# Kernel tuning notes

Hardware: AMD Instinct MI355X
Metric: run time of the kernel (lower is better)

The kernel has to match this reference:

```python
import jax, jax.numpy as jnp
import numpy as np
from functools import partial

STRIDES = (8, 16, 32)
SIZES = ((80, 80), (40, 40), (20, 20))
NUM_CLASSES = 80
NMS_THR = 0.65
SCORE_THR = 0.01
MAX_DET = 100  # fixed-size NMS output (padded; validity = scores > 0)


def setup_inputs() -> dict:
    key = jax.random.key(0)
    ks = jax.random.split(key, 9)
    B = 32
    out = {}
    for i, (h, w) in enumerate(SIZES):
        out[f"cls{i}"] = jax.random.normal(ks[3 * i], (B, NUM_CLASSES, h, w), jnp.float32)
        out[f"reg{i}"] = jax.random.normal(ks[3 * i + 1], (B, 4, h, w), jnp.float32)
        out[f"obj{i}"] = jax.random.normal(ks[3 * i + 2], (B, 1, h, w), jnp.float32)
    return out


def _grid_points():
    # MlvlPointGenerator.grid_priors(with_stride=True), offset=0: (x, y, stride, stride)
    pts = []
    for (h, w), s in zip(SIZES, STRIDES):
        xs = jnp.arange(w, dtype=jnp.float32) * s
        ys = jnp.arange(h, dtype=jnp.float32) * s
        xx, yy = jnp.meshgrid(xs, ys)  # [h, w], x varies fastest -> matches NHWC flatten
        st = jnp.full((h * w,), float(s), jnp.float32)
        pts.append(jnp.stack([xx.ravel(), yy.ravel(), st, st], axis=-1))
    return jnp.concatenate(pts, axis=0)  # [A, 4]


def _flatten(t, c):
    # [N, C, H, W] -> [N, H*W, C]  (permute(0,2,3,1).reshape)
    return t.transpose(0, 2, 3, 1).reshape(t.shape[0], -1, c)


def _decode(points, reg):
    # YOLOXBBoxDecoder: center = pred_xy * stride + point, wh = exp(pred_wh) * stride
    stride = points[:, 2:]                       # [A, 2]
    xys = reg[..., :2] * stride + points[:, :2]  # [B, A, 2]
    whs = jnp.exp(reg[..., 2:]) * stride         # [B, A, 2]
    return jnp.concatenate([xys - whs * 0.5, xys + whs * 0.5], axis=-1)  # x1y1x2y2


def _iou_one_vs_all(b, boxes):
    # b: [4], boxes: [A, 4]
    tl = jnp.maximum(b[:2], boxes[:, :2])
    br = jnp.minimum(b[2:], boxes[:, 2:])
    wh = jnp.clip(br - tl, 0.0)
    inter = wh[:, 0] * wh[:, 1]
    a1 = (b[2] - b[0]) * (b[3] - b[1])
    a2 = (boxes[:, 2] - boxes[:, 0]) * (boxes[:, 3] - boxes[:, 1])
    return inter / (a1 + a2 - inter + 1e-6)


def _nms_image(boxes, cls_scores, objectness):
    # boxes [A,4], cls_scores [A,C] (post-sigmoid), objectness [A] (post-sigmoid)
    max_scores = jnp.max(cls_scores, axis=1)
    labels = jnp.argmax(cls_scores, axis=1)
    scores = max_scores * objectness
    live = jnp.where(scores >= SCORE_THR, scores, -jnp.inf)  # score_thr filter

    # batched_nms: offset boxes per class so boxes of different labels never overlap
    offset = jax.lax.stop_gradient(jnp.max(jnp.abs(boxes)) + 1.0)
    boxes_off = jax.lax.stop_gradient(boxes) + labels.astype(boxes.dtype)[:, None] * offset

    def body(i, state):
        live, keep, kscores = state
        best = jnp.argmax(live)
        kscores = kscores.at[i].set(live[best])
        keep = keep.at[i].set(best)
        iou = _iou_one_vs_all(boxes_off[best], boxes_off)
        live = jnp.where(iou > NMS_THR, -jnp.inf, live)
        live = live.at[best].set(-jnp.inf)
        return live, keep, kscores

    keep0 = jnp.zeros((MAX_DET,), jnp.int32)
    ks0 = jnp.full((MAX_DET,), -jnp.inf, boxes.dtype)
    _, keep, kscores = jax.lax.fori_loop(0, MAX_DET, body, (live, keep0, ks0))

    valid = kscores > -jnp.inf
    out_boxes = jnp.where(valid[:, None], boxes[keep], 0.0)
    out_scores = jnp.where(valid, scores[keep], 0.0)
    out_labels = jnp.where(valid, labels[keep], -1)
    return out_boxes, out_scores, out_labels, valid


def _forward(cls0, cls1, cls2, reg0, reg1, reg2, obj0, obj1, obj2):
    B = cls0.shape[0]
    flat_cls = jax.nn.sigmoid(jnp.concatenate([_flatten(c, NUM_CLASSES) for c in (cls0, cls1, cls2)], axis=1))
    flat_reg = jnp.concatenate([_flatten(r, 4) for r in (reg0, reg1, reg2)], axis=1)
    flat_obj = jax.nn.sigmoid(jnp.concatenate([_flatten(o, 1) for o in (obj0, obj1, obj2)], axis=1))[..., 0]
    points = _grid_points()
    boxes = _decode(points, flat_reg)  # [B, A, 4]
    return jax.vmap(_nms_image)(boxes, flat_cls, flat_obj)


@jax.jit
def reference(cls0, cls1, cls2, reg0, reg1, reg2, obj0, obj1, obj2):
    return _forward(cls0, cls1, cls2, reg0, reg1, reg2, obj0, obj1, obj2)
```

## Files before the change

### kernel.cpp

```cpp
#include <hip/hip_runtime.h>
#include <cmath>

typedef unsigned int uint;
typedef unsigned long long ull;

#define BATCH 32
#define NA 8400
#define NC 80
#define MAXDET 100
#define NMSTHR 0.65f
#define SCTHR 0.01f
#define NEG_INF (-INFINITY)

#define NT 1024
#define NW (NT / 64)
#define EPT 9
#define NBINS 4096
#define CAP 512

__device__ __forceinline__ float stable_sigmoid(float x) {
    if (x >= 0.f) return 1.f / (1.f + expf(-x));
    float e = expf(x);
    return e / (1.f + e);
}

template<int HW, int W, int S>
__device__ __forceinline__ void decode4(
    const float* __restrict__ cls, const float* __restrict__ reg,
    const float* __restrict__ obj, int b, int p, int q, int ag,
    float4* __restrict__ wboxes, int* __restrict__ wlabels, uint* __restrict__ wkeys)
{
    const float* cbase = cls + (size_t)b * NC * HW + (size_t)(q * 20) * HW + p;
    float v[20];
    #pragma unroll
    for (int i = 0; i < 20; ++i) v[i] = cbase[(size_t)i * HW];
    float m = v[0]; int c = 0;
    #pragma unroll
    for (int i = 1; i < 20; ++i)
        if (v[i] > m) { m = v[i]; c = i; }
    c += q * 20;

    #pragma unroll
    for (int o = 1; o <= 2; o <<= 1) {
        float om = __shfl_xor(m, o);
        int   oc = __shfl_xor(c, o);
        if (om > m || (om == m && oc < c)) { m = om; c = oc; }
    }

    if (q == 0) {
        const float* rb = reg + (size_t)b * 4 * HW + p;
        float r0 = rb[0];
        float r1 = rb[HW];
        float r2 = rb[2 * (size_t)HW];
        float r3 = rb[3 * (size_t)HW];
        float ov = obj[(size_t)b * HW + p];

        int y = p / W;
        int x = p - y * W;
        float sc = stable_sigmoid(m) * stable_sigmoid(ov);
        float cx = r0 * (float)S + (float)x * (float)S;
        float cy = r1 * (float)S + (float)y * (float)S;
        float bw = expf(r2) * (float)S;
        float bh = expf(r3) * (float)S;

        wboxes[ag]  = make_float4(cx - bw * 0.5f, cy - bh * 0.5f,
                                  cx + bw * 0.5f, cy + bh * 0.5f);
        wlabels[ag] = c;
        wkeys[ag]   = (sc >= SCTHR) ? ~__float_as_uint(sc) : 0xFFFFFFFFu;
    }
}

__global__ __launch_bounds__(256) void decode_kernel(
    const float* __restrict__ cls0, const float* __restrict__ reg0, const float* __restrict__ obj0,
    const float* __restrict__ cls1, const float* __restrict__ reg1, const float* __restrict__ obj1,
    const float* __restrict__ cls2, const float* __restrict__ reg2, const float* __restrict__ obj2,
    float4* __restrict__ wboxes, int* __restrict__ wlabels, uint* __restrict__ wkeys)
{
    int gid = blockIdx.x * blockDim.x + threadIdx.x;
    int ag = gid >> 2;
    int q  = gid & 3;
    int b = ag / NA;
    int j = ag - b * NA;

    if (j < 6400)
        decode4<6400, 80, 8>(cls0, reg0, obj0, b, j, q, ag, wboxes, wlabels, wkeys);
    else if (j < 8000)
        decode4<1600, 40, 16>(cls1, reg1, obj1, b, j - 6400, q, ag, wboxes, wlabels, wkeys);
    else
        decode4<400, 20, 32>(cls2, reg2, obj2, b, j - 8000, q, ag, wboxes, wlabels, wkeys);
}

__global__ __launch_bounds__(NT) void nms_kernel(
    const float4* __restrict__ wboxes, const int* __restrict__ wlabels,
    const uint* __restrict__ wkeys, float* __restrict__ out)
{
    int b = blockIdx.x;
    int t = threadIdx.x;
    int lane = t & 63;
    int wv = t >> 6;
    const float4* boxes  = wboxes  + (size_t)b * NA;
    const int*    labels = wlabels + (size_t)b * NA;
    const uint*   keys   = wkeys   + (size_t)b * NA;

    __shared__ uint  s_hist[NBINS];
    __shared__ uint  s_cum[NBINS + 1];
    __shared__ uint  s_wsum[NW];
    __shared__ ull   s_skey[CAP];
    __shared__ float s_kbox[MAXDET][4];
    __shared__ float s_ka1[MAXDET];
    __shared__ int   s_kidx[MAXDET];
    __shared__ float s_kscr[MAXDET];
    __shared__ int   s_klab[MAXDET];
    __shared__ float s_red[NW];
    __shared__ float s_off;
    __shared__ int   s_kept, s_winlo, s_winhi, s_nsel;

    float m = 0.f;
    #pragma unroll
    for (int w = 0; w < EPT; ++w) {
        int e = t + w * NT;
        if (e < NA) {
            float4 v = boxes[e];
            m = fmaxf(m, fmaxf(fmaxf(fabsf(v.x), fabsf(v.y)),
                               fmaxf(fabsf(v.z), fabsf(v.w))));
        }
    }
    #pragma unroll
    for (int o = 32; o >= 1; o >>= 1) m = fmaxf(m, __shfl_xor(m, o));
    if (lane == 0) s_red[wv] = m;
    for (int i = t; i < NBINS; i += NT) s_hist[i] = 0;
    if (t == 0) { s_kept = 0; s_winlo = 0; }
    __syncthreads();
    if (t == 0) {
        float mm = 0.f;
        for (int w = 0; w < NW; ++w) mm = fmaxf(mm, s_red[w]);
        s_off = mm + 1.f;
    }
    #pragma unroll
    for (int w = 0; w < EPT; ++w) {
        int e = t + w * NT;
        if (e < NA) {
            uint k = keys[e];
            if (k != 0xFFFFFFFFu) atomicAdd(&s_hist[k >> 20], 1u);
        }
    }
    __syncthreads();
    float off = s_off;

    uint l0 = s_hist[4 * t], l1 = s_hist[4 * t + 1],
         l2 = s_hist[4 * t + 2], l3 = s_hist[4 * t + 3];
    uint L = l0 + l1 + l2 + l3;
    uint ls = L;
    #pragma unroll
    for (int o = 1; o < 64; o <<= 1) {
        uint v = __shfl_up(ls, o);
        if (lane >= o) ls += v;
    }
    if (lane == 63) s_wsum[wv] = ls;
    __syncthreads();
    if (t < NW) {
        uint v = s_wsum[t];
        uint vs = v;
        #pragma unroll
        for (int o = 1; o < NW; o <<= 1) {
            uint u = __shfl_up(vs, o);
            if ((t & 63) >= o) vs += u;
        }
        s_wsum[t] = vs - v;
    }
    __syncthreads();
    uint base = s_wsum[wv] + (ls - L);
    s_cum[4 * t]     = base;
    s_cum[4 * t + 1] = base + l0;
    s_cum[4 * t + 2] = base + l0 + l1;
    s_cum[4 * t + 3] = base + l0 + l1 + l2;
    if (t == NT - 1) s_cum[NBINS] = base + L;

    for (;;) {
        __syncthreads();
        int kept = s_kept, winlo = s_winlo;
        uint remaining = s_cum[NBINS] - s_cum[winlo];
        if (kept >= MAXDET || winlo >= NBINS || remaining == 0u) break;
        if (t == 0) { s_winhi = winlo + 1; s_nsel = 0; }
        if (t < CAP) s_skey[t] = ~0ull;
        __syncthreads();
        uint cl = s_cum[winlo];
        #pragma unroll
        for (int q = 0; q < 4; ++q) {
            int i = t + q * NT;
            if (i >= winlo && i < NBINS && (s_cum[i + 1] - cl) <= (uint)CAP)
                atomicMax(&s_winhi, i + 1);
        }
        __syncthreads();
        int winhi = s_winhi;

        #pragma unroll
        for (int w = 0; w < EPT; ++w) {
            int e = t + w * NT;
            bool q = false;
            uint k = 0;
            if (e < NA) {
                k = keys[e];
                if (k != 0xFFFFFFFFu) {
                    int bin = (int)(k >> 20);
                    q = (bin >= winlo && bin < winhi);
                }
            }
            ull mask = __ballot(q);
            if (mask) {
                int leader = __ffsll(mask) - 1;
                int pbase = 0;
                if (lane == leader) pbase = atomicAdd(&s_nsel, __popcll(mask));
                pbase = __shfl(pbase, leader);
                if (q) {
                    int pos = pbase + __popcll(mask & ((1ull << lane) - 1ull));
                    if (pos < CAP) s_skey[pos] = ((ull)k << 32) | (uint)e;
                }
            }
        }
        __syncthreads();
        int nsel = s_nsel; if (nsel > CAP) nsel = CAP;

        ull k = (t < CAP) ? s_skey[t] : ~0ull;
        for (int k2 = 2; k2 <= CAP; k2 <<= 1) {
            for (int j = k2 >> 1; j > 0; j >>= 1) {
                if (j >= 64) {
                    if (t < CAP) s_skey[t] = k;
                    __syncthreads();
                    if (t < CAP) {
                        ull kp = s_skey[t ^ j];
                        bool low = (t & j) == 0;
                        bool up  = (t & k2) == 0;
                        k = ((k < kp) == (low == up)) ? k : kp;
                    }
                    __syncthreads();
                } else if (t < CAP) {
                    ull kp = __shfl_xor(k, j);
                    bool low = (t & j) == 0;
                    bool up  = (t & k2) == 0;
                    k = ((k < kp) == (low == up)) ? k : kp;
                }
            }
        }
        if (t < CAP) s_skey[t] = k;
        __syncthreads();

        if (t < 64) {
            int kept2 = s_kept;
            for (int cb = 0; cb < nsel && kept2 < MAXDET; cb += 64) {
                int ci = cb + lane;
                ull sk = (ci < nsel) ? s_skey[ci] : ~0ull;
                bool has = (sk != ~0ull);
                int idx = 0, lab = 0;
                float sc = 0.f, c0 = 0.f, c1 = 0.f, c2 = 0.f, c3 = 0.f, ca = 0.f;
                if (has) {
                    idx = (int)(sk & 0xFFFFFFFFull);
                    sc  = __uint_as_float(~(uint)(sk >> 32));
                    float4 rb = boxes[idx];
                    lab = labels[idx];
                    float lo = (float)lab * off;
                    c0 = rb.x + lo; c1 = rb.y + lo; c2 = rb.z + lo; c3 = rb.w + lo;
                    ca = (c2 - c0) * (c3 - c1);
                    for (int q = 0; q < kept2; ++q) {
                        float tlx = fmaxf(s_kbox[q][0], c0);
                        float tly = fmaxf(s_kbox[q][1], c1);
                        float brx = fminf(s_kbox[q][2], c2);
                        float bry = fminf(s_kbox[q][3], c3);
                        float ww = fmaxf(brx - tlx, 0.f);
                        float hh = fmaxf(bry - tly, 0.f);
                        float inter = ww * hh;
                        float iou = inter / (s_ka1[q] + ca - inter + 1e-6f);
                        if (iou > NMSTHR) { has = false; break; }
                    }
                }
                ull am = __ballot(has);
                while (am && kept2 < MAXDET) {
                    int f = __ffsll(am) - 1;
                    float f0 = __shfl(c0, f), f1 = __shfl(c1, f);
                    float f2 = __shfl(c2, f), f3 = __shfl(c3, f);
                    float fa = __shfl(ca, f);
                    int   fidx = __shfl(idx, f);
                    int   flab = __shfl(lab, f);
                    float fsc  = __shfl(sc, f);
                    if (lane == 0) {
                        s_kbox[kept2][0] = f0; s_kbox[kept2][1] = f1;
                        s_kbox[kept2][2] = f2; s_kbox[kept2][3] = f3;
                        s_ka1[kept2] = fa; s_kidx[kept2] = fidx;
                        s_kscr[kept2] = fsc; s_klab[kept2] = flab;
                    }
                    kept2++;
                    if (lane == f) has = false;
                    if (has) {
                        float tlx = fmaxf(f0, c0), tly = fmaxf(f1, c1);
                        float brx = fminf(f2, c2), bry = fminf(f3, c3);
                        float ww = fmaxf(brx - tlx, 0.f), hh = fmaxf(bry - tly, 0.f);
                        float inter = ww * hh;
                        float iou = inter / (fa + ca - inter + 1e-6f);
                        if (iou > NMSTHR) has = false;
                    }
                    am = __ballot(has);
                }
            }
            if (lane == 0) s_kept = kept2;
        }
        __syncthreads();
        if (t == 0) s_winlo = s_winhi;
    }
    __syncthreads();

    if (t < MAXDET) {
        int kept = s_kept;
        float4 obx = make_float4(0.f, 0.f, 0.f, 0.f);
        float osc = 0.f, olab = -1.f, oval = 0.f;
        if (t < kept) {
            int idx = s_kidx[t];
            obx  = boxes[idx];
            osc  = s_kscr[t];
            olab = (float)s_klab[t];
            oval = 1.f;
        }
        float* ob = out + ((size_t)b * MAXDET + t) * 4;
        ob[0] = obx.x; ob[1] = obx.y; ob[2] = obx.z; ob[3] = obx.w;
        out[BATCH * MAXDET * 4 + b * MAXDET + t] = osc;
        out[BATCH * MAXDET * 5 + b * MAXDET + t] = olab;
        out[BATCH * MAXDET * 6 + b * MAXDET + t] = oval;
    }
}

extern "C" void kernel_launch(void* const* d_in, const int* in_sizes, int n_in,
                              void* d_out, int out_size, void* d_ws, size_t ws_size,
                              hipStream_t stream) {
    const float* cls0 = (const float*)d_in[0];
    const float* reg0 = (const float*)d_in[1];
    const float* obj0 = (const float*)d_in[2];
    const float* cls1 = (const float*)d_in[3];
    const float* reg1 = (const float*)d_in[4];
    const float* obj1 = (const float*)d_in[5];
    const float* cls2 = (const float*)d_in[6];
    const float* reg2 = (const float*)d_in[7];
    const float* obj2 = (const float*)d_in[8];

    char* ws = (char*)d_ws;
    size_t nBA = (size_t)BATCH * NA;
    float4* wboxes  = (float4*)ws;
    int*    wlabels = (int*)(ws + nBA * 16);
    uint*   wkeys   = (uint*)(ws + nBA * 20);

    int total = BATCH * NA * 4;
    decode_kernel<<<total / 256, 256, 0, stream>>>(
        cls0, reg0, obj0, cls1, reg1, obj1, cls2, reg2, obj2,
        wboxes, wlabels, wkeys);

    nms_kernel<<<BATCH, NT, 0, stream>>>(wboxes, wlabels, wkeys, (float*)d_out);
}
```

Measured before the change: 184.7 us.

## Fuse max-abs box reduction into decode and shrink NMS histogram to 256 bins

The decode kernel now computes the per-image maximum absolute box coordinate with wave and block reductions plus a global atomicMax, so the NMS kernel no longer rereads every box to find the label offset. The NMS histogram shrinks to 256 score bins over scores of roughly 2^-7 and above, which replaces the multi-wave prefix scan with a single-wave scan and removes the atomic window search. The NMS block also drops to 512 threads to match the sort capacity. Costs are an extra memset launch and more atomics in decode; coarser bins could pack more keys into one window, with overflow past CAP handled by the existing window loop.

```diff
diff --git a/kernel.cpp b/kernel.cpp
--- a/kernel.cpp
+++ b/kernel.cpp
@@ -12,10 +12,10 @@
 #define SCTHR 0.01f
 #define NEG_INF (-INFINITY)
 
-#define NT 1024
+#define NT 512
 #define NW (NT / 64)
-#define EPT 9
-#define NBINS 4096
+#define EPT 17
+#define NBINS 256
 #define CAP 512
 
 __device__ __forceinline__ float stable_sigmoid(float x) {
@@ -24,8 +24,15 @@
     return e / (1.f + e);
 }
 
+__device__ __forceinline__ int key2bin(uint k) {
+    uint sb = ~k;
+    uint s = (sb >= 0x3C000000u) ? ((sb - 0x3C000000u) >> 18) : 0u;
+    if (s > 255u) s = 255u;
+    return (int)(255u - s);
+}
+
 template<int HW, int W, int S>
-__device__ __forceinline__ void decode4(
+__device__ __forceinline__ float decode4(
     const float* __restrict__ cls, const float* __restrict__ reg,
     const float* __restrict__ obj, int b, int p, int q, int ag,
     float4* __restrict__ wboxes, int* __restrict__ wlabels, uint* __restrict__ wkeys)
@@ -47,6 +54,7 @@
         if (om > m || (om == m && oc < c)) { m = om; c = oc; }
     }
 
+    float mabs = 0.f;
     if (q == 0) {
         const float* rb = reg + (size_t)b * 4 * HW + p;
         float r0 = rb[0];
@@ -63,118 +71,121 @@
         float bw = expf(r2) * (float)S;
         float bh = expf(r3) * (float)S;
 
-        wboxes[ag]  = make_float4(cx - bw * 0.5f, cy - bh * 0.5f,
-                                  cx + bw * 0.5f, cy + bh * 0.5f);
+        float4 bx = make_float4(cx - bw * 0.5f, cy - bh * 0.5f,
+                                cx + bw * 0.5f, cy + bh * 0.5f);
+        wboxes[ag]  = bx;
         wlabels[ag] = c;
         wkeys[ag]   = (sc >= SCTHR) ? ~__float_as_uint(sc) : 0xFFFFFFFFu;
-    }
+        mabs = fmaxf(fmaxf(fabsf(bx.x), fabsf(bx.y)),
+                     fmaxf(fabsf(bx.z), fabsf(bx.w)));
+    }
+    return mabs;
 }
 
 __global__ __launch_bounds__(256) void decode_kernel(
     const float* __restrict__ cls0, const float* __restrict__ reg0, const float* __restrict__ obj0,
     const float* __restrict__ cls1, const float* __restrict__ reg1, const float* __restrict__ obj1,
     const float* __restrict__ cls2, const float* __restrict__ reg2, const float* __restrict__ obj2,
-    float4* __restrict__ wboxes, int* __restrict__ wlabels, uint* __restrict__ wkeys)
+    float4* __restrict__ wboxes, int* __restrict__ wlabels, uint* __restrict__ wkeys,
+    uint* __restrict__ wmaxabs)
 {
     int gid = blockIdx.x * blockDim.x + threadIdx.x;
     int ag = gid >> 2;
     int q  = gid & 3;
     int b = ag / NA;
     int j = ag - b * NA;
-
+    int lane = threadIdx.x & 63;
+    int wv = threadIdx.x >> 6;
+
+    float mabs;
     if (j < 6400)
-        decode4<6400, 80, 8>(cls0, reg0, obj0, b, j, q, ag, wboxes, wlabels, wkeys);
+        mabs = decode4<6400, 80, 8>(cls0, reg0, obj0, b, j, q, ag, wboxes, wlabels, wkeys);
     else if (j < 8000)
-        decode4<1600, 40, 16>(cls1, reg1, obj1, b, j - 6400, q, ag, wboxes, wlabels, wkeys);
+        mabs = decode4<1600, 40, 16>(cls1, reg1, obj1, b, j - 6400, q, ag, wboxes, wlabels, wkeys);
     else
-        decode4<400, 20, 32>(cls2, reg2, obj2, b, j - 8000, q, ag, wboxes, wlabels, wkeys);
+        mabs = decode4<400, 20, 32>(cls2, reg2, obj2, b, j - 8000, q, ag, wboxes, wlabels, wkeys);
+
+    __shared__ float s_lo[4], s_hi[4];
+    __shared__ int   s_b0[4], s_b63[4];
+    int b0 = __shfl(b, 0), b63 = __shfl(b, 63);
+    float mlo = (b == b0) ? mabs : 0.f;
+    float mhi = (b == b0) ? 0.f : mabs;
+    #pragma unroll
+    for (int o = 32; o >= 1; o >>= 1) {
+        mlo = fmaxf(mlo, __shfl_xor(mlo, o));
+        mhi = fmaxf(mhi, __shfl_xor(mhi, o));
+    }
+    if (lane == 0) { s_lo[wv] = mlo; s_hi[wv] = mhi; s_b0[wv] = b0; s_b63[wv] = b63; }
+    __syncthreads();
+    if (threadIdx.x == 0) {
+        int blo = s_b0[0], bhi = s_b63[3];
+        float vlo = 0.f, vhi = 0.f;
+        #pragma unroll
+        for (int w = 0; w < 4; ++w) {
+            vlo = fmaxf(vlo, (s_b0[w]  == blo) ? s_lo[w] : 0.f);
+            vlo = fmaxf(vlo, (s_b63[w] == blo) ? s_hi[w] : 0.f);
+            vhi = fmaxf(vhi, (s_b0[w]  == bhi) ? s_lo[w] : 0.f);
+            vhi = fmaxf(vhi, (s_b63[w] == bhi) ? s_hi[w] : 0.f);
+        }
+        atomicMax(&wmaxabs[blo], __float_as_uint(vlo));
+        if (bhi != blo) atomicMax(&wmaxabs[bhi], __float_as_uint(vhi));
+    }
 }
 
 __global__ __launch_bounds__(NT) void nms_kernel(
     const float4* __restrict__ wboxes, const int* __restrict__ wlabels,
-    const uint* __restrict__ wkeys, float* __restrict__ out)
+    const uint* __restrict__ wkeys, const uint* __restrict__ wmaxabs,
+    float* __restrict__ out)
 {
     int b = blockIdx.x;
     int t = threadIdx.x;
     int lane = t & 63;
-    int wv = t >> 6;
     const float4* boxes  = wboxes  + (size_t)b * NA;
     const int*    labels = wlabels + (size_t)b * NA;
     const uint*   keys   = wkeys   + (size_t)b * NA;
 
     __shared__ uint  s_hist[NBINS];
     __shared__ uint  s_cum[NBINS + 1];
-    __shared__ uint  s_wsum[NW];
     __shared__ ull   s_skey[CAP];
     __shared__ float s_kbox[MAXDET][4];
     __shared__ float s_ka1[MAXDET];
     __shared__ int   s_kidx[MAXDET];
     __shared__ float s_kscr[MAXDET];
     __shared__ int   s_klab[MAXDET];
-    __shared__ float s_red[NW];
-    __shared__ float s_off;
     __shared__ int   s_kept, s_winlo, s_winhi, s_nsel;
 
-    float m = 0.f;
-    #pragma unroll
-    for (int w = 0; w < EPT; ++w) {
-        int e = t + w * NT;
-        if (e < NA) {
-            float4 v = boxes[e];
-            m = fmaxf(m, fmaxf(fmaxf(fabsf(v.x), fabsf(v.y)),
-                               fmaxf(fabsf(v.z), fabsf(v.w))));
-        }
-    }
-    #pragma unroll
-    for (int o = 32; o >= 1; o >>= 1) m = fmaxf(m, __shfl_xor(m, o));
-    if (lane == 0) s_red[wv] = m;
-    for (int i = t; i < NBINS; i += NT) s_hist[i] = 0;
+    float off = __uint_as_float(wmaxabs[b]) + 1.f;
+
+    if (t < NBINS) s_hist[t] = 0;
     if (t == 0) { s_kept = 0; s_winlo = 0; }
     __syncthreads();
-    if (t == 0) {
-        float mm = 0.f;
-        for (int w = 0; w < NW; ++w) mm = fmaxf(mm, s_red[w]);
-        s_off = mm + 1.f;
-    }
     #pragma unroll
     for (int w = 0; w < EPT; ++w) {
         int e = t + w * NT;
         if (e < NA) {
             uint k = keys[e];
-            if (k != 0xFFFFFFFFu) atomicAdd(&s_hist[k >> 20], 1u);
+            if (k != 0xFFFFFFFFu) atomicAdd(&s_hist[key2bin(k)], 1u);
         }
     }
     __syncthreads();
-    float off = s_off;
-
-    uint l0 = s_hist[4 * t], l1 = s_hist[4 * t + 1],
-         l2 = s_hist[4 * t + 2], l3 = s_hist[4 * t + 3];
-    uint L = l0 + l1 + l2 + l3;
-    uint ls = L;
-    #pragma unroll
-    for (int o = 1; o < 64; o <<= 1) {
-        uint v = __shfl_up(ls, o);
-        if (lane >= o) ls += v;
-    }
-    if (lane == 63) s_wsum[wv] = ls;
-    __syncthreads();
-    if (t < NW) {
-        uint v = s_wsum[t];
-        uint vs = v;
+
+    if (t < 64) {
+        uint l0 = s_hist[4 * t], l1 = s_hist[4 * t + 1],
+             l2 = s_hist[4 * t + 2], l3 = s_hist[4 * t + 3];
+        uint L = l0 + l1 + l2 + l3;
+        uint ls = L;
         #pragma unroll
-        for (int o = 1; o < NW; o <<= 1) {
-            uint u = __shfl_up(vs, o);
-            if ((t & 63) >= o) vs += u;
-        }
-        s_wsum[t] = vs - v;
-    }
-    __syncthreads();
-    uint base = s_wsum[wv] + (ls - L);
-    s_cum[4 * t]     = base;
-    s_cum[4 * t + 1] = base + l0;
-    s_cum[4 * t + 2] = base + l0 + l1;
-    s_cum[4 * t + 3] = base + l0 + l1 + l2;
-    if (t == NT - 1) s_cum[NBINS] = base + L;
+        for (int o = 1; o < 64; o <<= 1) {
+            uint v = __shfl_up(ls, o);
+            if (lane >= o) ls += v;
+        }
+        uint base = ls - L;
+        s_cum[4 * t]     = base;
+        s_cum[4 * t + 1] = base + l0;
+        s_cum[4 * t + 2] = base + l0 + l1;
+        s_cum[4 * t + 3] = base + l0 + l1 + l2;
+        if (t == 63) s_cum[NBINS] = ls;
+    }
 
     for (;;) {
         __syncthreads();
@@ -182,14 +193,13 @@
         uint remaining = s_cum[NBINS] - s_cum[winlo];
         if (kept >= MAXDET || winlo >= NBINS || remaining == 0u) break;
         if (t == 0) { s_winhi = winlo + 1; s_nsel = 0; }
-        if (t < CAP) s_skey[t] = ~0ull;
+        s_skey[t] = ~0ull;
         __syncthreads();
         uint cl = s_cum[winlo];
-        #pragma unroll
-        for (int q = 0; q < 4; ++q) {
-            int i = t + q * NT;
-            if (i >= winlo && i < NBINS && (s_cum[i + 1] - cl) <= (uint)CAP)
-                atomicMax(&s_winhi, i + 1);
+        if (t >= winlo && t < NBINS) {
+            bool p0 = (s_cum[t + 1] - cl) <= (uint)CAP;
+            bool p1 = (t + 1 < NBINS) && ((s_cum[t + 2] - cl) <= (uint)CAP);
+            if (p0 && !p1) s_winhi = t + 1;
         }
         __syncthreads();
         int winhi = s_winhi;
@@ -202,7 +212,7 @@
             if (e < NA) {
                 k = keys[e];
                 if (k != 0xFFFFFFFFu) {
-                    int bin = (int)(k >> 20);
+                    int bin = key2bin(k);
                     q = (bin >= winlo && bin < winhi);
                 }
             }
@@ -221,20 +231,18 @@
         __syncthreads();
         int nsel = s_nsel; if (nsel > CAP) nsel = CAP;
 
-        ull k = (t < CAP) ? s_skey[t] : ~0ull;
+        ull k = s_skey[t];
         for (int k2 = 2; k2 <= CAP; k2 <<= 1) {
             for (int j = k2 >> 1; j > 0; j >>= 1) {
                 if (j >= 64) {
-                    if (t < CAP) s_skey[t] = k;
+                    s_skey[t] = k;
                     __syncthreads();
-                    if (t < CAP) {
-                        ull kp = s_skey[t ^ j];
-                        bool low = (t & j) == 0;
-                        bool up  = (t & k2) == 0;
-                        k = ((k < kp) == (low == up)) ? k : kp;
-                    }
+                    ull kp = s_skey[t ^ j];
+                    bool low = (t & j) == 0;
+                    bool up  = (t & k2) == 0;
+                    k = ((k < kp) == (low == up)) ? k : kp;
                     __syncthreads();
-                } else if (t < CAP) {
+                } else {
                     ull kp = __shfl_xor(k, j);
                     bool low = (t & j) == 0;
                     bool up  = (t & k2) == 0;
@@ -242,7 +250,7 @@
                 }
             }
         }
-        if (t < CAP) s_skey[t] = k;
+        s_skey[t] = k;
         __syncthreads();
 
         if (t < 64) {
@@ -345,11 +353,15 @@
     float4* wboxes  = (float4*)ws;
     int*    wlabels = (int*)(ws + nBA * 16);
     uint*   wkeys   = (uint*)(ws + nBA * 20);
+    uint*   wmaxabs = (uint*)(ws + nBA * 24);
+
+    hipMemsetAsync(wmaxabs, 0, BATCH * sizeof(uint), stream);
 
     int total = BATCH * NA * 4;
     decode_kernel<<<total / 256, 256, 0, stream>>>(
         cls0, reg0, obj0, cls1, reg1, obj1, cls2, reg2, obj2,
-        wboxes, wlabels, wkeys);
-
-    nms_kernel<<<BATCH, NT, 0, stream>>>(wboxes, wlabels, wkeys, (float*)d_out);
-}
+        wboxes, wlabels, wkeys, wmaxabs);
+
+    nms_kernel<<<BATCH, NT, 0, stream>>>(wboxes, wlabels, wkeys, wmaxabs,
+                                         (float*)d_out);
+}
```

After: 202.7 us. +9.7%, slower.
